# Performance work log

Hardware: AMD Instinct MI355X
Metric: run time of the kernel (lower is better)

## Reference

```python
import jax, jax.numpy as jnp
import numpy as np

B, G, N, D = 2, 2, 2048, 512
H, DH = 8, 64
DI = H * DH  # dim_inner = 512


def rmsnorm(x, gamma):
    # x: [b, g, n, d]; original normalizes over feature dim (F.normalize, eps=1e-12)
    norm = jnp.linalg.norm(x, axis=-1, keepdims=True)
    normed = x / jnp.maximum(norm, 1e-12)
    return normed * jnp.sqrt(jnp.asarray(x.shape[-1], x.dtype)) * gamma[None, :, None, :]


def setup_inputs() -> dict:
    key = jax.random.key(0)
    ks = jax.random.split(key, 8)
    x = jax.random.normal(ks[0], (B, G, N, D), dtype=jnp.float32)
    mask = jax.random.randint(ks[1], (B, N), 0, 2) > 0
    gamma_q = jnp.ones((G, D), dtype=jnp.float32)
    gamma_c = jnp.ones((G, D), dtype=jnp.float32)
    s = 0.02
    wq = jax.random.normal(ks[2], (G, DI, D), dtype=jnp.float32) * s
    wkv = jax.random.normal(ks[3], (G, 2 * DI, D), dtype=jnp.float32) * s
    wout = jax.random.normal(ks[4], (G, D, DI), dtype=jnp.float32) * s
    null_kv = jax.random.normal(ks[5], (2, G, H, 1, DH), dtype=jnp.float32)
    return {"x": x, "mask": mask, "gamma_q": gamma_q, "gamma_c": gamma_c,
            "wq": wq, "wkv": wkv, "wout": wout, "null_kv": null_kv}


def reference(x, mask, gamma_q, gamma_c, wq, wkv, wout, null_kv):
    b, g, n, d = x.shape
    # prenorm (context = x, so both norms applied to same input)
    xq = rmsnorm(x, gamma_q)
    xc = rmsnorm(x, gamma_c)
    # grouped 1x1 conv projections == per-group matmuls
    q = jnp.einsum('bgnd,ged->bgne', xq, wq)                 # [b,g,n,DI]
    kv = jnp.einsum('bgnd,ged->bgne', xc, wkv)               # [b,g,n,2*DI]
    k, v = jnp.split(kv, 2, axis=-1)
    def split_heads(t):
        return t.reshape(b, g, n, H, DH).transpose(0, 1, 3, 2, 4)  # [b,g,h,n,dh]
    q, k, v = map(split_heads, (q, k, v))
    # null kv: concat along sequence dim
    nk = jnp.broadcast_to(null_kv[0][None], (b, g, H, 1, DH))
    nv = jnp.broadcast_to(null_kv[1][None], (b, g, H, 1, DH))
    k = jnp.concatenate([nk, k], axis=-2)                    # [b,g,h,n+1,dh]
    v = jnp.concatenate([nv, v], axis=-2)
    # attention
    scale = DH ** -0.5
    scores = jnp.einsum('bghid,bghjd->bghij', q, k) * scale  # [b,g,h,n,n+1]
    m = jnp.concatenate([jnp.ones((b, 1), dtype=bool), mask], axis=-1)  # pad True for null kv
    scores = jnp.where(m[:, None, None, None, :], scores, jnp.asarray(-1e30, scores.dtype))
    attn = jax.nn.softmax(scores, axis=-1)
    out = jnp.einsum('bghij,bghjd->bghid', attn, v)          # [b,g,h,n,dh]
    out = out.transpose(0, 1, 3, 2, 4).reshape(b, g, n, DI)  # merge heads
    out = jnp.einsum('bgne,gde->bgnd', out, wout)
    return out
```

## Files before the change

kernel.cpp:

```cpp
#include <hip/hip_runtime.h>
#include <stdint.h>

typedef unsigned short u16;
typedef __attribute__((ext_vector_type(8))) short  bf16x8;
typedef __attribute__((ext_vector_type(8))) u16    u16x8;
typedef __attribute__((ext_vector_type(4))) u16    u16x4;
typedef __attribute__((ext_vector_type(4))) float  f32x4;
typedef __attribute__((ext_vector_type(16))) float f32x16;
typedef __attribute__((ext_vector_type(2))) unsigned u32x2;
typedef __attribute__((ext_vector_type(4))) unsigned u32x4;

#define SEQ 2048
#define DIM 512
#define NH  8
#define NBG 4
#define QSCALE 0.18033688011112042f

__device__ __forceinline__ float bf2f(u16 u) { return __uint_as_float(((unsigned)u) << 16); }
__device__ __forceinline__ u16 f2bf(float f) {
  unsigned u = __float_as_uint(f);
  return (u16)((u + 0x7FFFu + ((u >> 16) & 1u)) >> 16);
}
__device__ __forceinline__ float h2f(u16 u) { return (float)__builtin_bit_cast(_Float16, u); }
__device__ __forceinline__ u16 f2h(float f) { return __builtin_bit_cast(unsigned short, (_Float16)f); }

__device__ __forceinline__ float ex2(float x) {
#if __has_builtin(__builtin_amdgcn_exp2f)
  return __builtin_amdgcn_exp2f(x);
#else
  return exp2f(x);
#endif
}

__device__ __forceinline__ void gload_lds16(const void* g, void* l) {
#if __has_builtin(__builtin_amdgcn_global_load_lds)
  __builtin_amdgcn_global_load_lds((__attribute__((address_space(1))) void*)g,
                                   (__attribute__((address_space(3))) void*)l, 16, 0, 0);
#else
  *(u16x8*)l = *(const u16x8*)g;
#endif
}

__device__ __forceinline__ int float_mode(const void* gq) {
  unsigned w0 = *(const unsigned*)gq;
  return (w0 == 0x3F800000u) ? 1 : ((w0 == 0x3C003C00u) ? 2 : 0);
}
__device__ __forceinline__ int mask_mode(const void* maskp) {
  const unsigned* mw = (const unsigned*)maskp;
  bool all01 = true, lowhit = false, f32ish = true;
#pragma unroll
  for (int i = 0; i < 64; i++) {
    unsigned v = mw[i];
    all01 = all01 && (v <= 1u);
    lowhit = lowhit || ((v & 0xFFFFu) == 0x3F80u) || ((v & 0xFFFFu) == 0x3C00u);
    f32ish = f32ish && (v == 0u || v == 0x3F800000u);
  }
  return all01 ? 0 : (lowhit ? 1 : (f32ish ? 2 : 3));
}
__device__ __forceinline__ bool mask_at(const void* m, int idx, int mode) {
  if (mode == 0) return ((const int*)m)[idx] != 0;
  if (mode == 1) return ((const u16*)m)[idx] != 0;
  if (mode == 2) return ((const float*)m)[idx] != 0.f;
  return ((const unsigned char*)m)[idx] != 0;
}
__device__ __forceinline__ float ldf(const void* p, int i, int mode) {
  if (mode == 1) return ((const float*)p)[i];
  if (mode == 2) return h2f(((const u16*)p)[i]);
  return bf2f(((const u16*)p)[i]);
}

__global__ __launch_bounds__(256) void pre_kernel(
    const void* __restrict__ x, const void* __restrict__ gq, const void* __restrict__ gc,
    const void* __restrict__ wq, const void* __restrict__ wkv, const void* __restrict__ wout,
    const void* __restrict__ nkv, const void* __restrict__ maskp,
    u16* __restrict__ wqb, u16* __restrict__ wkvb, u16* __restrict__ woutb, u16* __restrict__ nkvb,
    u16* __restrict__ xn, int* __restrict__ gidx, int* __restrict__ nv)
{
  const int NWQ = 2*512*512, NWKV = 2*1024*512, NWOUT = 2*512*512;
  if (blockIdx.x >= 3073) {
    __shared__ int sc[2][256];
    __shared__ int tot;
    int b = blockIdx.x - 3073;
    int t = threadIdx.x;
    const int smode = mask_mode(maskp);
    int base = t * 8;
    int loc[8]; int c = 0;
#pragma unroll
    for (int i = 0; i < 8; i++) { loc[i] = mask_at(maskp, b * SEQ + base + i, smode) ? 1 : 0; c += loc[i]; }
    sc[0][t] = c;
    int src = 0, v = c;
    for (int off = 1; off < 256; off <<= 1) {
      __syncthreads();
      int add = (t >= off) ? sc[src][t - off] : 0;
      v += add;
      sc[src ^ 1][t] = v;
      src ^= 1;
    }
    int run = v - c;
#pragma unroll
    for (int i = 0; i < 8; i++) { if (loc[i]) gidx[b * SEQ + run] = base + i; run += loc[i]; }
    if (t == 255) { nv[b] = v; tot = v; }
    __syncthreads();
#pragma unroll
    for (int i = 0; i < 8; i++) {
      int p = base + i;
      if (p >= tot) gidx[b * SEQ + p] = 0;
    }
    return;
  }
  int mode = float_mode(gq);
  if (blockIdx.x < 1025) {
    int loc = (blockIdx.x * 256 + threadIdx.x) * 8;
    const void* s; u16* d; int fold = 0; const void* gam = nullptr; int gbase = 0; float ex = 1.f;
    if (loc < NWQ) { s = wq; d = wqb; fold = 1; gam = gq; gbase = ((loc >> 18) << 9) | (loc & 511); ex = QSCALE; }
    else { loc -= NWQ;
      if (loc < NWKV) { s = wkv; d = wkvb; fold = 1; gam = gc; gbase = ((loc >> 19) << 9) | (loc & 511); }
      else { loc -= NWKV;
        if (loc < NWOUT) { s = wout; d = woutb; }
        else { loc -= NWOUT; if (loc < 2048) { s = nkv; d = nkvb; } else return; } } }
    u16x8 o;
#pragma unroll
    for (int j = 0; j < 8; j++) {
      float v = ldf(s, loc + j, mode) * ex;
      if (fold) v *= ldf(gam, gbase + j, mode);
      o[j] = f2bf(v);
    }
    *(u16x8*)(d + loc) = o;
    return;
  }
  int row  = (blockIdx.x - 1025) * 4 + (threadIdx.x >> 6);
  int lane = threadIdx.x & 63;
  float f[8];
  if (mode == 1) {
    const float* xr = (const float*)x + (size_t)row * DIM + lane * 8;
    f32x4 a = *(const f32x4*)xr, b2 = *(const f32x4*)(xr + 4);
#pragma unroll
    for (int i = 0; i < 4; i++) { f[i] = a[i]; f[i + 4] = b2[i]; }
  } else if (mode == 2) {
    u16x8 v = *(const u16x8*)((const u16*)x + (size_t)row * DIM + lane * 8);
#pragma unroll
    for (int i = 0; i < 8; i++) f[i] = h2f(v[i]);
  } else {
    u16x8 v = *(const u16x8*)((const u16*)x + (size_t)row * DIM + lane * 8);
#pragma unroll
    for (int i = 0; i < 8; i++) f[i] = bf2f(v[i]);
  }
  float ss = 0.f;
#pragma unroll
  for (int i = 0; i < 8; i++) ss += f[i] * f[i];
#pragma unroll
  for (int off = 32; off; off >>= 1) ss += __shfl_xor(ss, off);
  float scale = 22.62741699796952f / fmaxf(sqrtf(ss), 1e-12f);
  u16x8 o;
#pragma unroll
  for (int i = 0; i < 8; i++) o[i] = f2bf(f[i] * scale);
  *(u16x8*)(xn + (size_t)row * DIM + lane * 8) = o;
}

__global__ __launch_bounds__(256, 4) void gemm_qkv(
    const u16* __restrict__ A, const u16* __restrict__ wqb, const u16* __restrict__ wkvb,
    u16* __restrict__ qb, u16* __restrict__ kb, u16* __restrict__ vtb,
    const int* __restrict__ gidx, const int* __restrict__ nv)
{
  __shared__ u16 As[128 * 64], Bs[64 * 64];
  int bg = blockIdx.z, g = bg & 1;
  int y = blockIdx.y;
  const u16* Bw; int Ncols, bn0, isq;
  if (y < 8) { Bw = wqb;  Ncols = 512;  bn0 = y * 64;       isq = 1; }
  else       { Bw = wkvb; Ncols = 1024; bn0 = (y - 8) * 64; isq = 0; }
  const int M = SEQ, K = DIM, ldc = 512;
  int bm0 = blockIdx.x * 128;
  if (!isq) {
    int nvb = nv[bg >> 1];
    if (bm0 >= ((nvb + 127) & ~127)) return;
  }
  int tid = threadIdx.x, w = tid >> 6, l = tid & 63;
  int li = l & 15, lg = l >> 4;
  int wr = w >> 1, wc = w & 1;
  const u16* Ab = A + (size_t)bg * M * K;
  const u16* Bb = Bw + (size_t)g * Ncols * K;
  int arow[4];
#pragma unroll
  for (int i = 0; i < 4; i++) {
    int r = bm0 + ((i * 256 + tid) >> 3);
    arow[i] = isq ? r : gidx[(bg >> 1) * SEQ + r];
  }
  f32x4 acc[4][2];
#pragma unroll
  for (int m = 0; m < 4; m++)
#pragma unroll
    for (int n = 0; n < 2; n++) acc[m][n] = (f32x4){0.f, 0.f, 0.f, 0.f};
  for (int kt = 0; kt < K; kt += 64) {
#pragma unroll
    for (int i = 0; i < 4; i++) {
      int ch = i * 256 + tid;
      gload_lds16(Ab + (size_t)arow[i] * K + kt + ((ch & 7) << 3), &As[ch * 8]);
    }
#pragma unroll
    for (int i = 0; i < 2; i++) {
      int ch = i * 256 + tid;
      gload_lds16(Bb + (size_t)(bn0 + (ch >> 3)) * K + kt + ((ch & 7) << 3), &Bs[ch * 8]);
    }
    __syncthreads();
#pragma unroll
    for (int kk = 0; kk < 2; kk++) {
      bf16x8 a[4], b[2];
#pragma unroll
      for (int m = 0; m < 4; m++) a[m] = *(const bf16x8*)&As[(wr * 64 + m * 16 + li) * 64 + kk * 32 + lg * 8];
#pragma unroll
      for (int n = 0; n < 2; n++) b[n] = *(const bf16x8*)&Bs[(wc * 32 + n * 16 + li) * 64 + kk * 32 + lg * 8];
      __builtin_amdgcn_s_setprio(1);
#pragma unroll
      for (int m = 0; m < 4; m++)
#pragma unroll
        for (int n = 0; n < 2; n++)
          acc[m][n] = __builtin_amdgcn_mfma_f32_16x16x32_bf16(a[m], b[n], acc[m][n], 0, 0, 0);
      __builtin_amdgcn_s_setprio(0);
    }
    __syncthreads();
  }
  if (isq) {
#pragma unroll
    for (int m = 0; m < 4; m++) {
#pragma unroll
      for (int n = 0; n < 2; n++) {
        int row = bm0 + wr * 64 + m * 16 + lg * 4;
        int col = bn0 + wc * 32 + n * 16 + li;
        u16* cp = qb + (size_t)bg * M * ldc + (size_t)row * ldc + col;
#pragma unroll
        for (int r = 0; r < 4; r++) cp[(size_t)r * ldc] = f2bf(acc[m][n][r]);
      }
    }
  } else {
#pragma unroll
    for (int m = 0; m < 4; m++) {
#pragma unroll
      for (int n = 0; n < 2; n++) {
        int row = bm0 + wr * 64 + m * 16 + lg * 4;
        int col = bn0 + wc * 32 + n * 16 + li;
        if (col < 512) {
          u16* cp = kb + (size_t)bg * M * ldc + (size_t)row * ldc + col;
#pragma unroll
          for (int r = 0; r < 4; r++) cp[(size_t)r * ldc] = f2bf(acc[m][n][r]);
        } else {
          u16x4 pk;
#pragma unroll
          for (int r = 0; r < 4; r++) pk[r] = f2bf(acc[m][n][r]);
          int prow = (row & ~12) | ((row & 4) << 1) | ((row & 8) >> 1);
          *(u16x4*)&vtb[(size_t)bg * 512 * M + (size_t)(col - 512) * M + prow] = pk;
        }
      }
    }
  }
}

__global__ __launch_bounds__(256, 4) void gemm_out(
    const u16* __restrict__ A, const u16* __restrict__ Bw,
    void* __restrict__ Cout, const void* __restrict__ gq0)
{
  __shared__ u16 As[128 * 64], Bs[64 * 64];
  const int M = SEQ, K = DIM, ldc = 512;
  int bg = blockIdx.z, g = bg & 1;
  int bm0 = blockIdx.x * 128, bn0 = blockIdx.y * 64;
  int tid = threadIdx.x, w = tid >> 6, l = tid & 63;
  int li = l & 15, lg = l >> 4;
  int wr = w >> 1, wc = w & 1;
  const u16* Ab = A + (size_t)bg * M * K;
  const u16* Bb = Bw + (size_t)g * 512 * K;
  f32x4 acc[4][2];
#pragma unroll
  for (int m = 0; m < 4; m++)
#pragma unroll
    for (int n = 0; n < 2; n++) acc[m][n] = (f32x4){0.f, 0.f, 0.f, 0.f};
  for (int kt = 0; kt < K; kt += 64) {
#pragma unroll
    for (int i = 0; i < 4; i++) {
      int ch = i * 256 + tid;
      gload_lds16(Ab + (size_t)(bm0 + (ch >> 3)) * K + kt + ((ch & 7) << 3), &As[ch * 8]);
    }
#pragma unroll
    for (int i = 0; i < 2; i++) {
      int ch = i * 256 + tid;
      gload_lds16(Bb + (size_t)(bn0 + (ch >> 3)) * K + kt + ((ch & 7) << 3), &Bs[ch * 8]);
    }
    __syncthreads();
#pragma unroll
    for (int kk = 0; kk < 2; kk++) {
      bf16x8 a[4], b[2];
#pragma unroll
      for (int m = 0; m < 4; m++) a[m] = *(const bf16x8*)&As[(wr * 64 + m * 16 + li) * 64 + kk * 32 + lg * 8];
#pragma unroll
      for (int n = 0; n < 2; n++) b[n] = *(const bf16x8*)&Bs[(wc * 32 + n * 16 + li) * 64 + kk * 32 + lg * 8];
      __builtin_amdgcn_s_setprio(1);
#pragma unroll
      for (int m = 0; m < 4; m++)
#pragma unroll
        for (int n = 0; n < 2; n++)
          acc[m][n] = __builtin_amdgcn_mfma_f32_16x16x32_bf16(a[m], b[n], acc[m][n], 0, 0, 0);
      __builtin_amdgcn_s_setprio(0);
    }
    __syncthreads();
  }
  int mode = float_mode(gq0);
#pragma unroll
  for (int m = 0; m < 4; m++) {
#pragma unroll
    for (int n = 0; n < 2; n++) {
      int row = bm0 + wr * 64 + m * 16 + lg * 4;
      int col = bn0 + wc * 32 + n * 16 + li;
      if (mode == 1) {
        float* cp = (float*)Cout + (size_t)bg * M * ldc + (size_t)row * ldc + col;
#pragma unroll
        for (int r = 0; r < 4; r++) cp[(size_t)r * ldc] = acc[m][n][r];
      } else if (mode == 2) {
        u16* cp = (u16*)Cout + (size_t)bg * M * ldc + (size_t)row * ldc + col;
#pragma unroll
        for (int r = 0; r < 4; r++) cp[(size_t)r * ldc] = f2h(acc[m][n][r]);
      } else {
        u16* cp = (u16*)Cout + (size_t)bg * M * ldc + (size_t)row * ldc + col;
#pragma unroll
        for (int r = 0; r < 4; r++) cp[(size_t)r * ldc] = f2bf(acc[m][n][r]);
      }
    }
  }
}

__global__ __launch_bounds__(256, 2) void attn_kernel(
    const u16* __restrict__ q, const u16* __restrict__ k, const u16* __restrict__ vt,
    const u16* __restrict__ nkv, const int* __restrict__ nv, u16* __restrict__ ao)
{
  __shared__ __align__(16) u16 Kb[2][64 * 64];
  __shared__ __align__(16) u16 Vb[2][64 * 64];
  const int bid = blockIdx.x;
  const int h = bid & 7, bg = (bid >> 3) & 3, ib = bid >> 5;
  const int g = bg & 1;
  const int tid = threadIdx.x, w = tid >> 6, l = tid & 63;
  const int lo = l & 31, hi = l >> 5;
  const int dl7 = lo & 7;
  const int i0 = ib * 128 + w * 32;
  const int nvb = nv[bg >> 1];
  const int NT = (nvb + 63) >> 6;

  auto stage = [&](int t, int buf) {
    int jb = t * 64;
#pragma unroll
    for (int p = 0; p < 2; p++) {
      int idx = p * 256 + tid;
      int r = idx >> 3, G = idx & 7;
      int c = (G ^ (r & 7)) << 3;
      gload_lds16(k + ((size_t)bg * SEQ + jb + r) * DIM + h * 64 + c, &Kb[buf][idx * 8]);
    }
#pragma unroll
    for (int p = 0; p < 2; p++) {
      int idx = p * 256 + tid;
      int r = idx >> 3, G = idx & 7;
      int c = (G ^ (r & 7)) << 3;
      gload_lds16(vt + ((size_t)bg * DIM + h * 64 + r) * SEQ + jb + c, &Vb[buf][idx * 8]);
    }
  };

  if (NT > 0) stage(0, 0);

  bf16x8 qf[4];
#pragma unroll
  for (int ks = 0; ks < 4; ks++)
    qf[ks] = *(const bf16x8*)&q[((size_t)bg * SEQ + i0 + lo) * DIM + h * 64 + ks * 16 + hi * 8];

  bf16x8 ones;
#pragma unroll
  for (int r = 0; r < 8; r++) ones[r] = (short)0x3F80;

  const u16* nk = nkv + ((size_t)g * NH + h) * 64;
  const u16* nvp = nkv + ((size_t)(2 + g) * NH + h) * 64;
  f32x16 oacc[2], lacc;
  {
    float s0 = 0.f;
#pragma unroll
    for (int ks = 0; ks < 4; ks++)
#pragma unroll
      for (int e = 0; e < 8; e++)
        s0 += bf2f((u16)qf[ks][e]) * bf2f(nk[ks * 16 + hi * 8 + e]);
    s0 += __shfl_xor(s0, 32);
    float pn = ex2(s0);
#pragma unroll
    for (int r = 0; r < 16; r++) lacc[r] = pn;
#pragma unroll
    for (int dblk = 0; dblk < 2; dblk++)
#pragma unroll
      for (int r = 0; r < 16; r++)
        oacc[dblk][r] = pn * bf2f(nvp[dblk * 32 + (r & 3) + 8 * (r >> 2) + 4 * hi]);
  }
  __syncthreads();

  for (int t = 0; t < NT; t++) {
    int cur = t & 1;
    if (t + 1 < NT) stage(t + 1, cur ^ 1);
    const bool tail = (t == NT - 1);
    const u16* kb = &Kb[cur][0];
    const u16* vb = &Vb[cur][0];

    bf16x8 vf[2][4];
#pragma unroll
    for (int dblk = 0; dblk < 2; dblk++)
#pragma unroll
      for (int f = 0; f < 4; f++) {
        int chunk = ((f * 2 + hi) ^ dl7) << 3;
        vf[dblk][f] = *(const bf16x8*)&vb[(dblk * 32 + lo) * 64 + chunk];
      }

    unsigned U[2][4][2];
#pragma unroll
    for (int jblk = 0; jblk < 2; jblk++) {
      f32x16 s;
#pragma unroll
      for (int r = 0; r < 16; r++) s[r] = 0.f;
      __builtin_amdgcn_s_setprio(1);
#pragma unroll
      for (int ks = 0; ks < 4; ks++) {
        bf16x8 kf = *(const bf16x8*)&kb[(jblk * 32 + lo) * 64 + (((ks * 2 + hi) ^ dl7) << 3)];
        s = __builtin_amdgcn_mfma_f32_32x32x16_bf16(kf, qf[ks], s, 0, 0, 0);
      }
      __builtin_amdgcn_s_setprio(0);
#pragma unroll
      for (int a = 0; a < 4; a++) {
        unsigned e0 = __float_as_uint(ex2(s[4 * a + 0]));
        unsigned e1 = __float_as_uint(ex2(s[4 * a + 1]));
        unsigned e2 = __float_as_uint(ex2(s[4 * a + 2]));
        unsigned e3 = __float_as_uint(ex2(s[4 * a + 3]));
        unsigned w01 = __builtin_amdgcn_perm(e1, e0, 0x07060302u);
        unsigned w23 = __builtin_amdgcn_perm(e3, e2, 0x07060302u);
        if (tail) {
          int j0 = t * 64 + jblk * 32 + 8 * a + 4 * hi;
          unsigned t01 = (j0 + 0 < nvb ? 0x0000FFFFu : 0u) | (j0 + 1 < nvb ? 0xFFFF0000u : 0u);
          unsigned t23 = (j0 + 2 < nvb ? 0x0000FFFFu : 0u) | (j0 + 3 < nvb ? 0xFFFF0000u : 0u);
          w01 &= t01; w23 &= t23;
        }
        U[jblk][a][0] = w01;
        U[jblk][a][1] = w23;
      }
    }
    __builtin_amdgcn_s_setprio(1);
#pragma unroll
    for (int jblk = 0; jblk < 2; jblk++)
#pragma unroll
      for (int m = 0; m < 2; m++) {
        bf16x8 pf = __builtin_bit_cast(bf16x8,
          (u32x4){U[jblk][2 * m][0], U[jblk][2 * m][1], U[jblk][2 * m + 1][0], U[jblk][2 * m + 1][1]});
        lacc    = __builtin_amdgcn_mfma_f32_32x32x16_bf16(ones, pf, lacc, 0, 0, 0);
        oacc[0] = __builtin_amdgcn_mfma_f32_32x32x16_bf16(vf[0][jblk * 2 + m], pf, oacc[0], 0, 0, 0);
        oacc[1] = __builtin_amdgcn_mfma_f32_32x32x16_bf16(vf[1][jblk * 2 + m], pf, oacc[1], 0, 0, 0);
      }
    __builtin_amdgcn_s_setprio(0);
    __syncthreads();
  }

  float inv = 1.f / lacc[0];
#pragma unroll
  for (int dblk = 0; dblk < 2; dblk++)
#pragma unroll
    for (int rq = 0; rq < 4; rq++) {
      u16x4 o;
#pragma unroll
      for (int qq = 0; qq < 4; qq++) o[qq] = f2bf(oacc[dblk][4 * rq + qq] * inv);
      *(u16x4*)&ao[((size_t)bg * SEQ + i0 + lo) * DIM + h * 64 + dblk * 32 + 8 * rq + 4 * hi] = o;
    }
}

extern "C" void kernel_launch(void* const* d_in, const int* in_sizes, int n_in,
                              void* d_out, int out_size, void* d_ws, size_t ws_size,
                              hipStream_t stream) {
  const void* x    = d_in[0];
  const void* msk  = d_in[1];
  const void* gq   = d_in[2];
  const void* gc   = d_in[3];
  const void* wq   = d_in[4];
  const void* wkv  = d_in[5];
  const void* wout = d_in[6];
  const void* nkv  = d_in[7];

  u16* base = (u16*)d_ws;
  const size_t SLOT = (size_t)NBG * SEQ * DIM;
  u16* xn = base + 0 * SLOT;
  u16* ao = base + 0 * SLOT;
  u16* qb = base + 1 * SLOT;
  u16* kb = base + 2 * SLOT;
  u16* vt = base + 3 * SLOT;
  u16* wreg = base + 4 * SLOT;
  const int NWQ = 2 * 512 * 512, NWKV = 2 * 1024 * 512, NWOUT = 2 * 512 * 512;
  u16* wqb   = wreg;
  u16* wkvb  = wreg + NWQ;
  u16* woutb = wreg + NWQ + NWKV;
  u16* nkvb  = wreg + NWQ + NWKV + NWOUT;
  int* gidx  = (int*)(nkvb + 2048);
  int* nv    = gidx + 2 * SEQ;

  hipLaunchKernelGGL(pre_kernel, dim3(3075), dim3(256), 0, stream,
                     x, gq, gc, wq, wkv, wout, nkv, msk,
                     wqb, wkvb, woutb, nkvb, xn, gidx, nv);
  hipLaunchKernelGGL(gemm_qkv, dim3(16, 24, NBG), dim3(256), 0, stream,
                     xn, wqb, wkvb, qb, kb, vt, gidx, nv);
  hipLaunchKernelGGL(attn_kernel, dim3(512), dim3(256), 0, stream,
                     qb, kb, vt, nkvb, nv, ao);
  hipLaunchKernelGGL(gemm_out, dim3(16, 8, NBG), dim3(256), 0, stream,
                     ao, woutb, d_out, gq);
}
```

Baseline: 84.71 us.

## Split attention KV range across waves with per-wave pipelines and LDS reduction

The attention kernel changes from four waves each owning 32 query rows over the full KV range to four waves sharing 64 query rows, with each wave taking every fourth 32-key tile. Each wave runs its own double-buffered async K/V staging using vmcnt waits instead of block-wide barriers, and the partial numerators and denominators are combined through LDS at the end. The grid doubles to 1024 blocks. This removes per-tile __syncthreads and raises parallelism, at the cost of a cross-wave reduction, more LDS, and a scalar-strided output store.

```diff
diff --git a/kernel.cpp b/kernel.cpp
--- a/kernel.cpp
+++ b/kernel.cpp
@@ -327,100 +327,121 @@
 
 __global__ __launch_bounds__(256, 2) void attn_kernel(
     const u16* __restrict__ q, const u16* __restrict__ k, const u16* __restrict__ vt,
-    const u16* __restrict__ nkv, const int* __restrict__ nv, u16* __restrict__ ao)
+    const u16* __restrict__ nkv, const int* __restrict__ nvcnt, u16* __restrict__ ao)
 {
-  __shared__ __align__(16) u16 Kb[2][64 * 64];
-  __shared__ __align__(16) u16 Vb[2][64 * 64];
+  __shared__ __align__(16) u16 smem[32768];
   const int bid = blockIdx.x;
   const int h = bid & 7, bg = (bid >> 3) & 3, ib = bid >> 5;
   const int g = bg & 1;
   const int tid = threadIdx.x, w = tid >> 6, l = tid & 63;
   const int lo = l & 31, hi = l >> 5;
-  const int dl7 = lo & 7;
-  const int i0 = ib * 128 + w * 32;
-  const int nvb = nv[bg >> 1];
-  const int NT = (nvb + 63) >> 6;
-
-  auto stage = [&](int t, int buf) {
-    int jb = t * 64;
-#pragma unroll
-    for (int p = 0; p < 2; p++) {
-      int idx = p * 256 + tid;
-      int r = idx >> 3, G = idx & 7;
-      int c = (G ^ (r & 7)) << 3;
-      gload_lds16(k + ((size_t)bg * SEQ + jb + r) * DIM + h * 64 + c, &Kb[buf][idx * 8]);
-    }
-#pragma unroll
-    for (int p = 0; p < 2; p++) {
-      int idx = p * 256 + tid;
-      int r = idx >> 3, G = idx & 7;
-      int c = (G ^ (r & 7)) << 3;
-      gload_lds16(vt + ((size_t)bg * DIM + h * 64 + r) * SEQ + jb + c, &Vb[buf][idx * 8]);
+  const int dl7 = lo & 7, dl3 = lo & 3;
+  const int i0 = ib * 64;
+  const int nvb = nvcnt[bg >> 1];
+  const int NT32 = (nvb + 31) >> 5;
+  const int myNT = (NT32 > w) ? ((NT32 - w + 3) >> 2) : 0;
+  const int wb = w * 8192;
+
+  bf16x8 qf[2][4];
+#pragma unroll
+  for (int it = 0; it < 2; it++)
+#pragma unroll
+    for (int ks = 0; ks < 4; ks++)
+      qf[it][ks] = *(const bf16x8*)&q[((size_t)bg * SEQ + i0 + it * 32 + lo) * DIM + h * 64 + ks * 16 + hi * 8];
+
+  auto stage = [&](int t, int b) {
+    int jb = t * 32;
+    u16* kd = &smem[wb + b * 4096];
+    u16* vd = kd + 2048;
+#pragma unroll
+    for (int p = 0; p < 4; p++) {
+      int idx = p * 64 + l;
+      int row = idx >> 3, G = idx & 7;
+      gload_lds16(k + ((size_t)bg * SEQ + jb + row) * DIM + h * 64 + ((G ^ (row & 7)) << 3), &kd[idx * 8]);
+    }
+#pragma unroll
+    for (int p = 0; p < 4; p++) {
+      int idx = p * 64 + l;
+      int d = idx >> 2, G = idx & 3;
+      gload_lds16(vt + ((size_t)bg * DIM + h * 64 + d) * SEQ + jb + ((G ^ (d & 3)) << 3), &vd[idx * 8]);
     }
   };
 
-  if (NT > 0) stage(0, 0);
-
-  bf16x8 qf[4];
-#pragma unroll
-  for (int ks = 0; ks < 4; ks++)
-    qf[ks] = *(const bf16x8*)&q[((size_t)bg * SEQ + i0 + lo) * DIM + h * 64 + ks * 16 + hi * 8];
+  if (myNT > 0) stage(w, 0);
+  if (myNT > 1) stage(w + 4, 1);
 
   bf16x8 ones;
 #pragma unroll
   for (int r = 0; r < 8; r++) ones[r] = (short)0x3F80;
 
-  const u16* nk = nkv + ((size_t)g * NH + h) * 64;
+  const u16* nk  = nkv + ((size_t)g * NH + h) * 64;
   const u16* nvp = nkv + ((size_t)(2 + g) * NH + h) * 64;
-  f32x16 oacc[2], lacc;
-  {
-    float s0 = 0.f;
+  f32x16 oaccA[2], oaccB[2], laccA, laccB;
+#pragma unroll
+  for (int r = 0; r < 16; r++) { laccA[r] = 0.f; laccB[r] = 0.f; }
+#pragma unroll
+  for (int dblk = 0; dblk < 2; dblk++)
+#pragma unroll
+    for (int r = 0; r < 16; r++) { oaccA[dblk][r] = 0.f; oaccB[dblk][r] = 0.f; }
+  if (w == 0) {
+#pragma unroll
+    for (int it = 0; it < 2; it++) {
+      float s0 = 0.f;
+#pragma unroll
+      for (int ks = 0; ks < 4; ks++)
+#pragma unroll
+        for (int e = 0; e < 8; e++)
+          s0 += bf2f((u16)qf[it][ks][e]) * bf2f(nk[ks * 16 + hi * 8 + e]);
+      s0 += __shfl_xor(s0, 32);
+      float pn = ex2(s0);
+      f32x16& la = it ? laccB : laccA;
+#pragma unroll
+      for (int r = 0; r < 16; r++) la[r] = pn;
+#pragma unroll
+      for (int dblk = 0; dblk < 2; dblk++) {
+        f32x16& oa = it ? oaccB[dblk] : oaccA[dblk];
+#pragma unroll
+        for (int r = 0; r < 16; r++)
+          oa[r] = pn * bf2f(nvp[dblk * 32 + (r & 3) + 8 * (r >> 2) + 4 * hi]);
+      }
+    }
+  }
+
+  for (int i = 0; i < myNT; i++) {
+    int t = w + 4 * i;
+    int b = i & 1;
+    if (i + 1 < myNT) asm volatile("s_waitcnt vmcnt(8)" ::: "memory");
+    else              asm volatile("s_waitcnt vmcnt(0)" ::: "memory");
+    __builtin_amdgcn_sched_barrier(0);
+    const u16* kbuf = &smem[wb + b * 4096];
+    const u16* vbuf = kbuf + 2048;
+
+    bf16x8 kf[4], vf[2][2];
 #pragma unroll
     for (int ks = 0; ks < 4; ks++)
-#pragma unroll
-      for (int e = 0; e < 8; e++)
-        s0 += bf2f((u16)qf[ks][e]) * bf2f(nk[ks * 16 + hi * 8 + e]);
-    s0 += __shfl_xor(s0, 32);
-    float pn = ex2(s0);
-#pragma unroll
-    for (int r = 0; r < 16; r++) lacc[r] = pn;
+      kf[ks] = *(const bf16x8*)&kbuf[(lo * 8 + (((ks * 2 + hi) ^ dl7))) * 8];
 #pragma unroll
     for (int dblk = 0; dblk < 2; dblk++)
 #pragma unroll
-      for (int r = 0; r < 16; r++)
-        oacc[dblk][r] = pn * bf2f(nvp[dblk * 32 + (r & 3) + 8 * (r >> 2) + 4 * hi]);
-  }
-  __syncthreads();
-
-  for (int t = 0; t < NT; t++) {
-    int cur = t & 1;
-    if (t + 1 < NT) stage(t + 1, cur ^ 1);
-    const bool tail = (t == NT - 1);
-    const u16* kb = &Kb[cur][0];
-    const u16* vb = &Vb[cur][0];
-
-    bf16x8 vf[2][4];
-#pragma unroll
-    for (int dblk = 0; dblk < 2; dblk++)
-#pragma unroll
-      for (int f = 0; f < 4; f++) {
-        int chunk = ((f * 2 + hi) ^ dl7) << 3;
-        vf[dblk][f] = *(const bf16x8*)&vb[(dblk * 32 + lo) * 64 + chunk];
-      }
-
-    unsigned U[2][4][2];
-#pragma unroll
-    for (int jblk = 0; jblk < 2; jblk++) {
+      for (int jm = 0; jm < 2; jm++)
+        vf[dblk][jm] = *(const bf16x8*)&vbuf[((dblk * 32 + lo) * 4 + (((jm * 2 + hi) ^ dl3))) * 8];
+    asm volatile("s_waitcnt lgkmcnt(0)" ::: "memory");
+    __builtin_amdgcn_sched_barrier(0);
+    if (i + 2 < myNT) stage(w + 4 * (i + 2), b);
+    __builtin_amdgcn_sched_barrier(0);
+
+    const bool tail = (t == NT32 - 1);
+#pragma unroll
+    for (int it = 0; it < 2; it++) {
       f32x16 s;
 #pragma unroll
       for (int r = 0; r < 16; r++) s[r] = 0.f;
       __builtin_amdgcn_s_setprio(1);
 #pragma unroll
-      for (int ks = 0; ks < 4; ks++) {
-        bf16x8 kf = *(const bf16x8*)&kb[(jblk * 32 + lo) * 64 + (((ks * 2 + hi) ^ dl7) << 3)];
-        s = __builtin_amdgcn_mfma_f32_32x32x16_bf16(kf, qf[ks], s, 0, 0, 0);
-      }
+      for (int ks = 0; ks < 4; ks++)
+        s = __builtin_amdgcn_mfma_f32_32x32x16_bf16(kf[ks], qf[it][ks], s, 0, 0, 0);
       __builtin_amdgcn_s_setprio(0);
+      unsigned U[4][2];
 #pragma unroll
       for (int a = 0; a < 4; a++) {
         unsigned e0 = __float_as_uint(ex2(s[4 * a + 0]));
@@ -430,40 +451,61 @@
         unsigned w01 = __builtin_amdgcn_perm(e1, e0, 0x07060302u);
         unsigned w23 = __builtin_amdgcn_perm(e3, e2, 0x07060302u);
         if (tail) {
-          int j0 = t * 64 + jblk * 32 + 8 * a + 4 * hi;
+          int j0 = t * 32 + 8 * a + 4 * hi;
           unsigned t01 = (j0 + 0 < nvb ? 0x0000FFFFu : 0u) | (j0 + 1 < nvb ? 0xFFFF0000u : 0u);
           unsigned t23 = (j0 + 2 < nvb ? 0x0000FFFFu : 0u) | (j0 + 3 < nvb ? 0xFFFF0000u : 0u);
           w01 &= t01; w23 &= t23;
         }
-        U[jblk][a][0] = w01;
-        U[jblk][a][1] = w23;
-      }
-    }
-    __builtin_amdgcn_s_setprio(1);
-#pragma unroll
-    for (int jblk = 0; jblk < 2; jblk++)
+        U[a][0] = w01; U[a][1] = w23;
+      }
+      f32x16& la = it ? laccB : laccA;
+      f32x16& o0 = it ? oaccB[0] : oaccA[0];
+      f32x16& o1 = it ? oaccB[1] : oaccA[1];
+      __builtin_amdgcn_s_setprio(1);
 #pragma unroll
       for (int m = 0; m < 2; m++) {
         bf16x8 pf = __builtin_bit_cast(bf16x8,
-          (u32x4){U[jblk][2 * m][0], U[jblk][2 * m][1], U[jblk][2 * m + 1][0], U[jblk][2 * m + 1][1]});
-        lacc    = __builtin_amdgcn_mfma_f32_32x32x16_bf16(ones, pf, lacc, 0, 0, 0);
-        oacc[0] = __builtin_amdgcn_mfma_f32_32x32x16_bf16(vf[0][jblk * 2 + m], pf, oacc[0], 0, 0, 0);
-        oacc[1] = __builtin_amdgcn_mfma_f32_32x32x16_bf16(vf[1][jblk * 2 + m], pf, oacc[1], 0, 0, 0);
-      }
-    __builtin_amdgcn_s_setprio(0);
+          (u32x4){U[2 * m][0], U[2 * m][1], U[2 * m + 1][0], U[2 * m + 1][1]});
+        la = __builtin_amdgcn_mfma_f32_32x32x16_bf16(ones, pf, la, 0, 0, 0);
+        o0 = __builtin_amdgcn_mfma_f32_32x32x16_bf16(vf[0][m], pf, o0, 0, 0, 0);
+        o1 = __builtin_amdgcn_mfma_f32_32x32x16_bf16(vf[1][m], pf, o1, 0, 0, 0);
+      }
+      __builtin_amdgcn_s_setprio(0);
+    }
+  }
+
+#pragma unroll
+  for (int pass = 0; pass < 2; pass++) {
+    if (pass) __syncthreads();
+    float* Psw = (float*)&smem[wb];
+    float* Lsw = (float*)&smem[wb + 4096];
+    const f32x16* oa = pass ? oaccB : oaccA;
+    const f32x16& la = pass ? laccB : laccA;
+#pragma unroll
+    for (int dblk = 0; dblk < 2; dblk++)
+#pragma unroll
+      for (int r = 0; r < 16; r++) {
+        int d = dblk * 32 + (r & 3) + 8 * (r >> 2) + 4 * hi;
+        Psw[d * 32 + lo] = oa[dblk][r];
+      }
+    if (hi == 0) Lsw[lo] = la[0];
     __syncthreads();
-  }
-
-  float inv = 1.f / lacc[0];
-#pragma unroll
-  for (int dblk = 0; dblk < 2; dblk++)
-#pragma unroll
-    for (int rq = 0; rq < 4; rq++) {
-      u16x4 o;
-#pragma unroll
-      for (int qq = 0; qq < 4; qq++) o[qq] = f2bf(oacc[dblk][4 * rq + qq] * inv);
-      *(u16x4*)&ao[((size_t)bg * SEQ + i0 + lo) * DIM + h * 64 + dblk * 32 + 8 * rq + 4 * hi] = o;
-    }
+#pragma unroll
+    for (int rep = 0; rep < 2; rep++) {
+      int qi = rep * 256 + tid;
+      int d = qi >> 3, i4 = (qi & 7) << 2;
+      f32x4 sum = (f32x4){0.f, 0.f, 0.f, 0.f};
+      f32x4 lq  = (f32x4){0.f, 0.f, 0.f, 0.f};
+#pragma unroll
+      for (int w2 = 0; w2 < 4; w2++) {
+        sum += *(const f32x4*)((const float*)&smem[w2 * 8192] + d * 32 + i4);
+        lq  += *(const f32x4*)((const float*)&smem[w2 * 8192 + 4096] + i4);
+      }
+#pragma unroll
+      for (int e = 0; e < 4; e++)
+        ao[((size_t)bg * SEQ + i0 + pass * 32 + i4 + e) * DIM + h * 64 + d] = f2bf(sum[e] / lq[e]);
+    }
+  }
 }
 
 extern "C" void kernel_launch(void* const* d_in, const int* in_sizes, int n_in,
@@ -499,7 +541,7 @@
                      wqb, wkvb, woutb, nkvb, xn, gidx, nv);
   hipLaunchKernelGGL(gemm_qkv, dim3(16, 24, NBG), dim3(256), 0, stream,
                      xn, wqb, wkvb, qb, kb, vt, gidx, nv);
-  hipLaunchKernelGGL(attn_kernel, dim3(512), dim3(256), 0, stream,
+  hipLaunchKernelGGL(attn_kernel, dim3(1024), dim3(256), 0, stream,
                      qb, kb, vt, nkvb, nv, ao);
   hipLaunchKernelGGL(gemm_out, dim3(16, 8, NBG), dim3(256), 0, stream,
                      ao, woutb, d_out, gq);
```

Measured after the change: 93.63 us. +10.5%, slower.
